# Performance work log

Measured on AMD Instinct MI355X. Metric: run time of the kernel, lower is better.

## Reference

```python
import jax, jax.numpy as jnp
import numpy as np

N_NODES = 100_000
N_EDGES = 1_000_000
VOCAB = 10_000
HID = 75
OUT = 64
BN_EPS = 1e-5


def gcn_conv(x, edge_index, W, b, n):
    # PyG GCNConv: add self-loops, symmetric deg^{-1/2} normalization, then scatter-add.
    loop = jnp.arange(n, dtype=edge_index.dtype)
    src = jnp.concatenate([edge_index[0], loop])
    dst = jnp.concatenate([edge_index[1], loop])
    deg = jax.ops.segment_sum(jnp.ones_like(src, dtype=x.dtype), dst, num_segments=n)
    dinv = jnp.where(deg > 0, jax.lax.rsqrt(deg), 0.0)
    norm = dinv[src] * dinv[dst]              # [E+N]
    h = x @ W                                  # linear before propagate (PyG order)
    msg = h[src] * norm[:, None]               # gather + per-edge scale
    out = jax.ops.segment_sum(msg, dst, num_segments=n)
    return out + b


def batch_norm(x, gamma, beta):
    # BatchNorm1d over nodes, training mode (biased variance)
    mu = jnp.mean(x, axis=0)
    var = jnp.mean(jnp.square(x - mu), axis=0)
    return (x - mu) * jax.lax.rsqrt(var + BN_EPS) * gamma + beta


def setup_inputs() -> dict:
    key = jax.random.key(0)
    ks = jax.random.split(key, 8)
    x = jax.random.randint(ks[0], (N_NODES,), 0, VOCAB, dtype=jnp.int64)
    edge_index = jax.random.randint(ks[1], (2, N_EDGES), 0, N_NODES, dtype=jnp.int64)
    emb = jax.random.normal(ks[2], (VOCAB, HID), dtype=jnp.float32)
    scale = 1.0 / np.sqrt(HID)
    Ws = jax.random.normal(ks[3], (4, HID, HID), dtype=jnp.float32) * scale
    bs = jnp.zeros((4, HID), dtype=jnp.float32)
    gammas = jnp.ones((4, HID), dtype=jnp.float32)
    betas = jnp.zeros((4, HID), dtype=jnp.float32)
    W_mu = jax.random.normal(ks[4], (HID, OUT), dtype=jnp.float32) * scale
    b_mu = jnp.zeros((OUT,), dtype=jnp.float32)
    W_logstd = jax.random.normal(ks[5], (HID, OUT), dtype=jnp.float32) * scale
    b_logstd = jnp.zeros((OUT,), dtype=jnp.float32)
    return {"x": x, "edge_index": edge_index, "emb": emb, "Ws": Ws, "bs": bs,
            "gammas": gammas, "betas": betas, "W_mu": W_mu, "b_mu": b_mu,
            "W_logstd": W_logstd, "b_logstd": b_logstd}


def reference(x, edge_index, emb, Ws, bs, gammas, betas, W_mu, b_mu, W_logstd, b_logstd):
    h = emb[x]  # [N, 75] embedding lookup
    for i in range(4):
        h = jax.nn.relu(batch_norm(gcn_conv(h, edge_index, Ws[i], bs[i], N_NODES), gammas[i], betas[i]))
    mu = gcn_conv(h, edge_index, W_mu, b_mu, N_NODES)
    logstd = gcn_conv(h, edge_index, W_logstd, b_logstd, N_NODES)
    return (mu, logstd)
```

## Files before the change

kernel.cpp:

```cpp
#include <hip/hip_runtime.h>

#define NN 100000
#define NE 1000000
#define HID 75
#define SP 80
#define OUTF 64
#define BN_EPS 1e-5f
#define KP 104

#define SCAN_ELEMS 1024
#define SCAN_NBLK ((NN + SCAN_ELEMS - 1) / SCAN_ELEMS)

typedef short bf16x8 __attribute__((ext_vector_type(8)));
typedef float f32x4  __attribute__((ext_vector_type(4)));

__device__ __forceinline__ ushort f2bf(float f) {
    unsigned u = __float_as_uint(f);
    u += 0x7FFF + ((u >> 16) & 1);
    return (ushort)(u >> 16);
}
__device__ __forceinline__ float bf_lo(unsigned u) { return __uint_as_float(u << 16); }
__device__ __forceinline__ float bf_hi(unsigned u) { return __uint_as_float(u & 0xFFFF0000u); }

__global__ void hist_kernel(const int* __restrict__ dst, int* __restrict__ hist, int E) {
    int e = blockIdx.x * blockDim.x + threadIdx.x;
    if (e < E) atomicAdd(&hist[dst[e]], 1);
}

__global__ void dinv_kernel(const int* __restrict__ hist, float* __restrict__ dinv, int n) {
    int i = blockIdx.x * blockDim.x + threadIdx.x;
    if (i < n) dinv[i] = rsqrtf((float)hist[i] + 1.0f);
}

__global__ void scan_pass1(const int* __restrict__ hist, int* __restrict__ bsum) {
    __shared__ int sdata[256];
    int base = blockIdx.x * SCAN_ELEMS;
    int t = threadIdx.x;
    int s = 0;
    #pragma unroll
    for (int k = 0; k < 4; ++k) {
        int i = base + t * 4 + k;
        if (i < NN) s += hist[i];
    }
    sdata[t] = s;
    __syncthreads();
    for (int off = 128; off > 0; off >>= 1) {
        if (t < off) sdata[t] += sdata[t + off];
        __syncthreads();
    }
    if (t == 0) bsum[blockIdx.x] = sdata[0];
}

__global__ void scan_pass2(int* __restrict__ bsum, int* __restrict__ row_ptr, int nblk) {
    if (threadIdx.x == 0) {
        int acc = 0;
        for (int i = 0; i < nblk; ++i) { int v = bsum[i]; bsum[i] = acc; acc += v; }
        row_ptr[NN] = acc;
    }
}

__global__ void scan_pass3(const int* __restrict__ hist, const int* __restrict__ bsum,
                           int* __restrict__ row_ptr) {
    __shared__ int sdata[256];
    int base = blockIdx.x * SCAN_ELEMS;
    int t = threadIdx.x;
    int v[4];
    int s = 0;
    #pragma unroll
    for (int k = 0; k < 4; ++k) {
        int i = base + t * 4 + k;
        v[k] = (i < NN) ? hist[i] : 0;
        s += v[k];
    }
    sdata[t] = s;
    __syncthreads();
    for (int off = 1; off < 256; off <<= 1) {
        int x = (t >= off) ? sdata[t - off] : 0;
        __syncthreads();
        sdata[t] += x;
        __syncthreads();
    }
    int pre = bsum[blockIdx.x] + sdata[t] - s;
    #pragma unroll
    for (int k = 0; k < 4; ++k) {
        int i = base + t * 4 + k;
        if (i < NN) { row_ptr[i] = pre; pre += v[k]; }
    }
}

__global__ void csr_fill(const int* __restrict__ src, const int* __restrict__ dst,
                         const int* __restrict__ row_ptr, int* __restrict__ cnt,
                         int* __restrict__ col, int E) {
    int e = blockIdx.x * blockDim.x + threadIdx.x;
    if (e >= E) return;
    int d = dst[e];
    int slot = row_ptr[d] + atomicAdd(&cnt[d], 1);
    col[slot] = src[e];
}

__global__ void embed_kernel(const int* __restrict__ x, const float* __restrict__ emb,
                             float* __restrict__ h) {
    int t = blockIdx.x * blockDim.x + threadIdx.x;
    if (t >= NN * SP) return;
    int node = t / SP, f = t % SP;
    h[t] = (f < HID) ? emb[x[node] * HID + f] : 0.0f;
}

template<int J, bool BNRELU>
__global__ __launch_bounds__(256, 2)
void gemm_mfma(const float* __restrict__ h, const float* __restrict__ W,
               const float* __restrict__ ab, const float* __restrict__ dinv,
               ushort* __restrict__ outb) {
    constexpr int NT = (J + 15) / 16;
    constexpr int JP = NT * 16;
    constexpr int OS = JP;
    __shared__ ushort Wl[JP * KP];
    __shared__ ushort Hl[64 * KP];
    int tl = threadIdx.x;
    int rbase = blockIdx.x * 64;
    for (int idx = tl; idx < 96 * JP; idx += 256) {
        int k = idx / JP, n = idx % JP;
        float v = (k < HID && n < J) ? W[k * J + n] : 0.0f;
        Wl[n * KP + k] = f2bf(v);
    }
    for (int idx = tl; idx < 64 * 20; idx += 256) {
        int r = idx / 20, c = idx % 20;
        int row = rbase + r; if (row >= NN) row = NN - 1;
        float4 v = reinterpret_cast<const float4*>(h + (size_t)row * SP)[c];
        if (BNRELU) {
            float4 a4 = reinterpret_cast<const float4*>(ab)[c];
            float4 c4 = reinterpret_cast<const float4*>(ab + SP)[c];
            v.x = fmaxf(fmaf(v.x, a4.x, c4.x), 0.f);
            v.y = fmaxf(fmaf(v.y, a4.y, c4.y), 0.f);
            v.z = fmaxf(fmaf(v.z, a4.z, c4.z), 0.f);
            v.w = fmaxf(fmaf(v.w, a4.w, c4.w), 0.f);
        }
        ushort4 u;
        u.x = f2bf(v.x); u.y = f2bf(v.y); u.z = f2bf(v.z); u.w = f2bf(v.w);
        *reinterpret_cast<ushort4*>(&Hl[r * KP + c * 4]) = u;
    }
    for (int idx = tl; idx < 64 * 16; idx += 256) {
        int r = idx / 16, k = 80 + (idx % 16);
        Hl[r * KP + k] = 0;
    }
    __syncthreads();
    int w = tl >> 6;
    int l = tl & 63;
    int cq = l & 15;
    int q  = l >> 4;
    f32x4 acc[NT] = {};
    #pragma unroll
    for (int ks = 0; ks < 3; ++ks) {
        int k0 = ks * 32 + q * 8;
        bf16x8 a = *reinterpret_cast<const bf16x8*>(&Hl[(w * 16 + cq) * KP + k0]);
        #pragma unroll
        for (int t = 0; t < NT; ++t) {
            bf16x8 b = *reinterpret_cast<const bf16x8*>(&Wl[(t * 16 + cq) * KP + k0]);
            acc[t] = __builtin_amdgcn_mfma_f32_16x16x32_bf16(a, b, acc[t], 0, 0, 0);
        }
    }
    int r0 = rbase + w * 16 + q * 4;
    #pragma unroll
    for (int r = 0; r < 4; ++r) {
        int grow = r0 + r;
        if (grow < NN) {
            float d = dinv[grow];
            ushort* orow = outb + (size_t)grow * OS;
            #pragma unroll
            for (int t = 0; t < NT; ++t)
                orow[t * 16 + cq] = f2bf(acc[t][r] * d);
        }
    }
}

#define ACCUM(W) \
    a0 += bf_lo(W.x); a1 += bf_hi(W.x); a2 += bf_lo(W.y); a3 += bf_hi(W.y);

__global__ void gather75(const int* __restrict__ row_ptr, const int* __restrict__ col,
                         const uint2* __restrict__ hWb, const float* __restrict__ dinv,
                         float* __restrict__ agg) {
    int t = blockIdx.x * 256 + threadIdx.x;
    if (t >= NN * 20) return;
    int n = t / 20, c = t % 20;
    int beg = row_ptr[n], end = row_ptr[n + 1];
    uint2 v = hWb[(size_t)n * 20 + c];
    float a0 = bf_lo(v.x), a1 = bf_hi(v.x), a2 = bf_lo(v.y), a3 = bf_hi(v.y);
    int e = beg;
    for (; e + 3 < end; e += 4) {
        int s0 = col[e], s1 = col[e + 1], s2 = col[e + 2], s3 = col[e + 3];
        uint2 w0 = hWb[(size_t)s0 * 20 + c];
        uint2 w1 = hWb[(size_t)s1 * 20 + c];
        uint2 w2 = hWb[(size_t)s2 * 20 + c];
        uint2 w3 = hWb[(size_t)s3 * 20 + c];
        ACCUM(w0) ACCUM(w1) ACCUM(w2) ACCUM(w3)
    }
    for (; e < end; ++e) {
        uint2 w0 = hWb[(size_t)col[e] * 20 + c];
        ACCUM(w0)
    }
    float d = dinv[n];
    reinterpret_cast<float4*>(agg)[(size_t)n * 20 + c] =
        make_float4(a0 * d, a1 * d, a2 * d, a3 * d);
}

__global__ void gather64(const int* __restrict__ row_ptr, const int* __restrict__ col,
                         const uint2* __restrict__ hWb, const float* __restrict__ dinv,
                         const float* __restrict__ bias, float* __restrict__ out) {
    int t = blockIdx.x * 256 + threadIdx.x;
    int n = t / 16, c = t % 16;
    int beg = row_ptr[n], end = row_ptr[n + 1];
    uint2 v = hWb[(size_t)n * 16 + c];
    float a0 = bf_lo(v.x), a1 = bf_hi(v.x), a2 = bf_lo(v.y), a3 = bf_hi(v.y);
    int e = beg;
    for (; e + 3 < end; e += 4) {
        int s0 = col[e], s1 = col[e + 1], s2 = col[e + 2], s3 = col[e + 3];
        uint2 w0 = hWb[(size_t)s0 * 16 + c];
        uint2 w1 = hWb[(size_t)s1 * 16 + c];
        uint2 w2 = hWb[(size_t)s2 * 16 + c];
        uint2 w3 = hWb[(size_t)s3 * 16 + c];
        ACCUM(w0) ACCUM(w1) ACCUM(w2) ACCUM(w3)
    }
    for (; e < end; ++e) {
        uint2 w0 = hWb[(size_t)col[e] * 16 + c];
        ACCUM(w0)
    }
    float d = dinv[n];
    float4 b = *reinterpret_cast<const float4*>(bias + c * 4);
    reinterpret_cast<float4*>(out)[(size_t)n * 16 + c] =
        make_float4(fmaf(a0, d, b.x), fmaf(a1, d, b.y), fmaf(a2, d, b.z), fmaf(a3, d, b.w));
}

__global__ void stats_kernel(const float* __restrict__ agg, float* __restrict__ stats) {
    __shared__ float ssum[SP], ssq[SP];
    if (threadIdx.x < SP) { ssum[threadIdx.x] = 0.f; ssq[threadIdx.x] = 0.f; }
    __syncthreads();
    int gtid = blockIdx.x * blockDim.x + threadIdx.x;
    int T = gridDim.x * blockDim.x;
    int c = gtid % 20;
    int r = gtid / 20;
    int rstep = T / 20;
    float4 s = make_float4(0.f, 0.f, 0.f, 0.f), q = make_float4(0.f, 0.f, 0.f, 0.f);
    for (; r < NN; r += rstep) {
        float4 v = reinterpret_cast<const float4*>(agg)[r * 20 + c];
        s.x += v.x; s.y += v.y; s.z += v.z; s.w += v.w;
        q.x += v.x * v.x; q.y += v.y * v.y; q.z += v.z * v.z; q.w += v.w * v.w;
    }
    atomicAdd(&ssum[c * 4 + 0], s.x); atomicAdd(&ssum[c * 4 + 1], s.y);
    atomicAdd(&ssum[c * 4 + 2], s.z); atomicAdd(&ssum[c * 4 + 3], s.w);
    atomicAdd(&ssq[c * 4 + 0], q.x); atomicAdd(&ssq[c * 4 + 1], q.y);
    atomicAdd(&ssq[c * 4 + 2], q.z); atomicAdd(&ssq[c * 4 + 3], q.w);
    __syncthreads();
    if (threadIdx.x < SP) {
        atomicAdd(&stats[threadIdx.x], ssum[threadIdx.x]);
        atomicAdd(&stats[SP + threadIdx.x], ssq[threadIdx.x]);
    }
}

__global__ void bn_finalize(const float* __restrict__ stats, const float* __restrict__ gamma,
                            const float* __restrict__ beta, float* __restrict__ ab) {
    int f = threadIdx.x;
    if (f >= SP) return;
    float a = 0.f, cc = 0.f;
    if (f < HID) {
        float mu = stats[f] * (1.0f / NN);
        float var = stats[SP + f] * (1.0f / NN) - mu * mu;
        a = gamma[f] * rsqrtf(var + BN_EPS);
        cc = beta[f] - mu * a;
    }
    ab[f] = a;
    ab[SP + f] = cc;
}

extern "C" void kernel_launch(void* const* d_in, const int* in_sizes, int n_in,
                              void* d_out, int out_size, void* d_ws, size_t ws_size,
                              hipStream_t stream) {
    const int*   x      = (const int*)d_in[0];
    const int*   ei     = (const int*)d_in[1];
    const float* emb    = (const float*)d_in[2];
    const float* Ws     = (const float*)d_in[3];
    const float* gammas = (const float*)d_in[5];
    const float* betas  = (const float*)d_in[6];
    const float* W_mu   = (const float*)d_in[7];
    const float* b_mu   = (const float*)d_in[8];
    const float* W_ls   = (const float*)d_in[9];
    const float* b_ls   = (const float*)d_in[10];
    float* out = (float*)d_out;

    const int E = in_sizes[1] / 2;
    const int* src = ei;
    const int* dst = ei + E;

    char* ws = (char*)d_ws;
    float*  dinv    = (float*) (ws + 0);
    float*  stats   = (float*) (ws + 400000);
    float*  ab      = (float*) (ws + 400640);
    int*    hist    = (int*)   (ws + 401408);
    int*    row_ptr = (int*)   (ws + 801408);
    int*    cnt     = (int*)   (ws + 1201536);
    int*    bsum    = (int*)   (ws + 1601536);
    int*    col     = (int*)   (ws + 1602048);
    float*  hA      = (float*) (ws + 5602048);
    ushort* hBb     = (ushort*)(ws + 37602048);

    hipMemsetAsync(hist, 0, NN * sizeof(int), stream);
    hist_kernel<<<(E + 255) / 256, 256, 0, stream>>>(dst, hist, E);
    dinv_kernel<<<(NN + 255) / 256, 256, 0, stream>>>(hist, dinv, NN);
    scan_pass1<<<SCAN_NBLK, 256, 0, stream>>>(hist, bsum);
    scan_pass2<<<1, 64, 0, stream>>>(bsum, row_ptr, SCAN_NBLK);
    scan_pass3<<<SCAN_NBLK, 256, 0, stream>>>(hist, bsum, row_ptr);
    hipMemsetAsync(cnt, 0, NN * sizeof(int), stream);
    csr_fill<<<(E + 255) / 256, 256, 0, stream>>>(src, dst, row_ptr, cnt, col, E);

    embed_kernel<<<(NN * SP + 255) / 256, 256, 0, stream>>>(x, emb, hA);

    for (int layer = 0; layer < 4; ++layer) {
        const float* W = Ws + (size_t)layer * HID * HID;
        if (layer == 0)
            gemm_mfma<HID, false><<<(NN + 63) / 64, 256, 0, stream>>>(hA, W, ab, dinv, hBb);
        else
            gemm_mfma<HID, true><<<(NN + 63) / 64, 256, 0, stream>>>(hA, W, ab, dinv, hBb);
        gather75<<<(NN * 20 + 255) / 256, 256, 0, stream>>>(row_ptr, col, (const uint2*)hBb, dinv, hA);
        hipMemsetAsync(stats, 0, 2 * SP * sizeof(float), stream);
        stats_kernel<<<640, 256, 0, stream>>>(hA, stats);
        bn_finalize<<<1, 128, 0, stream>>>(stats, gammas + layer * HID, betas + layer * HID, ab);
    }

    gemm_mfma<OUTF, true><<<(NN + 63) / 64, 256, 0, stream>>>(hA, W_mu, ab, dinv, hBb);
    gather64<<<(NN * 16) / 256, 256, 0, stream>>>(row_ptr, col, (const uint2*)hBb, dinv, b_mu, out);

    float* out2 = out + (size_t)NN * OUTF;
    gemm_mfma<OUTF, true><<<(NN + 63) / 64, 256, 0, stream>>>(hA, W_ls, ab, dinv, hBb);
    gather64<<<(NN * 16) / 256, 256, 0, stream>>>(row_ptr, col, (const uint2*)hBb, dinv, b_ls, out2);
}
```

Before: 628.7 us.

## Degree-sort nodes for gather load balance and fuse mu/logstd heads

Builds a permutation of nodes bucketed by in-degree (a counting sort on capped degree) and has the gather kernels visit nodes in that order, so lanes in a wavefront work on rows of similar length and divergence drops. It also merges the two output heads into one GEMM with a 128-wide concatenated weight and a single 128-feature gather that writes both outputs, removing one GEMM and one gather pass. The cost is a few extra setup kernels, scattered output writes under the permutation, and a wider intermediate buffer.

```diff
diff --git a/kernel.cpp b/kernel.cpp
--- a/kernel.cpp
+++ b/kernel.cpp
@@ -96,6 +96,42 @@
     int d = dst[e];
     int slot = row_ptr[d] + atomicAdd(&cnt[d], 1);
     col[slot] = src[e];
+}
+
+__global__ void deg_hist_kernel(const int* __restrict__ hist, int* __restrict__ dh) {
+    __shared__ int lh[64];
+    if (threadIdx.x < 64) lh[threadIdx.x] = 0;
+    __syncthreads();
+    int i = blockIdx.x * 256 + threadIdx.x;
+    if (i < NN) atomicAdd(&lh[min(hist[i], 63)], 1);
+    __syncthreads();
+    if (threadIdx.x < 64 && lh[threadIdx.x]) atomicAdd(&dh[threadIdx.x], lh[threadIdx.x]);
+}
+
+__global__ void deg_scan_kernel(const int* __restrict__ dh, int* __restrict__ doff) {
+    if (threadIdx.x == 0) {
+        int acc = 0;
+        for (int d = 0; d < 64; ++d) { doff[d] = acc; acc += dh[d]; }
+    }
+}
+
+__global__ void perm_fill_kernel(const int* __restrict__ hist, int* __restrict__ doff,
+                                 int* __restrict__ perm) {
+    __shared__ int lcnt[64];
+    __shared__ int gbase[64];
+    if (threadIdx.x < 64) lcnt[threadIdx.x] = 0;
+    __syncthreads();
+    int i = blockIdx.x * 256 + threadIdx.x;
+    int d = 0, lrank = 0;
+    bool act = (i < NN);
+    if (act) { d = min(hist[i], 63); lrank = atomicAdd(&lcnt[d], 1); }
+    __syncthreads();
+    if (threadIdx.x < 64) {
+        int c = lcnt[threadIdx.x];
+        gbase[threadIdx.x] = c ? atomicAdd(&doff[threadIdx.x], c) : 0;
+    }
+    __syncthreads();
+    if (act) perm[gbase[d] + lrank] = i;
 }
 
 __global__ void embed_kernel(const int* __restrict__ x, const float* __restrict__ emb,
@@ -173,15 +209,81 @@
     }
 }
 
+__global__ __launch_bounds__(256, 2)
+void gemm_mfma_dual(const float* __restrict__ h, const float* __restrict__ Wmu,
+                    const float* __restrict__ Wls, const float* __restrict__ ab,
+                    const float* __restrict__ dinv, ushort* __restrict__ outb) {
+    constexpr int NT = 8;
+    constexpr int JP = 128;
+    __shared__ ushort Wl[JP * KP];
+    __shared__ ushort Hl[64 * KP];
+    int tl = threadIdx.x;
+    int rbase = blockIdx.x * 64;
+    for (int idx = tl; idx < 96 * JP; idx += 256) {
+        int k = idx / JP, n = idx % JP;
+        float v = 0.f;
+        if (k < HID) v = (n < 64) ? Wmu[k * 64 + n] : Wls[k * 64 + (n - 64)];
+        Wl[n * KP + k] = f2bf(v);
+    }
+    for (int idx = tl; idx < 64 * 20; idx += 256) {
+        int r = idx / 20, c = idx % 20;
+        int row = rbase + r; if (row >= NN) row = NN - 1;
+        float4 v = reinterpret_cast<const float4*>(h + (size_t)row * SP)[c];
+        float4 a4 = reinterpret_cast<const float4*>(ab)[c];
+        float4 c4 = reinterpret_cast<const float4*>(ab + SP)[c];
+        v.x = fmaxf(fmaf(v.x, a4.x, c4.x), 0.f);
+        v.y = fmaxf(fmaf(v.y, a4.y, c4.y), 0.f);
+        v.z = fmaxf(fmaf(v.z, a4.z, c4.z), 0.f);
+        v.w = fmaxf(fmaf(v.w, a4.w, c4.w), 0.f);
+        ushort4 u;
+        u.x = f2bf(v.x); u.y = f2bf(v.y); u.z = f2bf(v.z); u.w = f2bf(v.w);
+        *reinterpret_cast<ushort4*>(&Hl[r * KP + c * 4]) = u;
+    }
+    for (int idx = tl; idx < 64 * 16; idx += 256) {
+        int r = idx / 16, k = 80 + (idx % 16);
+        Hl[r * KP + k] = 0;
+    }
+    __syncthreads();
+    int w = tl >> 6;
+    int l = tl & 63;
+    int cq = l & 15;
+    int q  = l >> 4;
+    f32x4 acc[NT] = {};
+    #pragma unroll
+    for (int ks = 0; ks < 3; ++ks) {
+        int k0 = ks * 32 + q * 8;
+        bf16x8 a = *reinterpret_cast<const bf16x8*>(&Hl[(w * 16 + cq) * KP + k0]);
+        #pragma unroll
+        for (int t = 0; t < NT; ++t) {
+            bf16x8 b = *reinterpret_cast<const bf16x8*>(&Wl[(t * 16 + cq) * KP + k0]);
+            acc[t] = __builtin_amdgcn_mfma_f32_16x16x32_bf16(a, b, acc[t], 0, 0, 0);
+        }
+    }
+    int r0 = rbase + w * 16 + q * 4;
+    #pragma unroll
+    for (int r = 0; r < 4; ++r) {
+        int grow = r0 + r;
+        if (grow < NN) {
+            float d = dinv[grow];
+            ushort* orow = outb + (size_t)grow * 128;
+            #pragma unroll
+            for (int t = 0; t < NT; ++t)
+                orow[t * 16 + cq] = f2bf(acc[t][r] * d);
+        }
+    }
+}
+
 #define ACCUM(W) \
     a0 += bf_lo(W.x); a1 += bf_hi(W.x); a2 += bf_lo(W.y); a3 += bf_hi(W.y);
 
 __global__ void gather75(const int* __restrict__ row_ptr, const int* __restrict__ col,
+                         const int* __restrict__ perm,
                          const uint2* __restrict__ hWb, const float* __restrict__ dinv,
                          float* __restrict__ agg) {
     int t = blockIdx.x * 256 + threadIdx.x;
     if (t >= NN * 20) return;
-    int n = t / 20, c = t % 20;
+    int n = perm[t / 20];
+    int c = t % 20;
     int beg = row_ptr[n], end = row_ptr[n + 1];
     uint2 v = hWb[(size_t)n * 20 + c];
     float a0 = bf_lo(v.x), a1 = bf_hi(v.x), a2 = bf_lo(v.y), a3 = bf_hi(v.y);
@@ -203,30 +305,36 @@
         make_float4(a0 * d, a1 * d, a2 * d, a3 * d);
 }
 
-__global__ void gather64(const int* __restrict__ row_ptr, const int* __restrict__ col,
-                         const uint2* __restrict__ hWb, const float* __restrict__ dinv,
-                         const float* __restrict__ bias, float* __restrict__ out) {
+__global__ void gather128(const int* __restrict__ row_ptr, const int* __restrict__ col,
+                          const int* __restrict__ perm,
+                          const uint2* __restrict__ hWb, const float* __restrict__ dinv,
+                          const float* __restrict__ b_mu, const float* __restrict__ b_ls,
+                          float* __restrict__ out_mu, float* __restrict__ out_ls) {
     int t = blockIdx.x * 256 + threadIdx.x;
-    int n = t / 16, c = t % 16;
+    int n = perm[t >> 5];
+    int c = t & 31;
     int beg = row_ptr[n], end = row_ptr[n + 1];
-    uint2 v = hWb[(size_t)n * 16 + c];
+    uint2 v = hWb[(size_t)n * 32 + c];
     float a0 = bf_lo(v.x), a1 = bf_hi(v.x), a2 = bf_lo(v.y), a3 = bf_hi(v.y);
     int e = beg;
     for (; e + 3 < end; e += 4) {
         int s0 = col[e], s1 = col[e + 1], s2 = col[e + 2], s3 = col[e + 3];
-        uint2 w0 = hWb[(size_t)s0 * 16 + c];
-        uint2 w1 = hWb[(size_t)s1 * 16 + c];
-        uint2 w2 = hWb[(size_t)s2 * 16 + c];
-        uint2 w3 = hWb[(size_t)s3 * 16 + c];
+        uint2 w0 = hWb[(size_t)s0 * 32 + c];
+        uint2 w1 = hWb[(size_t)s1 * 32 + c];
+        uint2 w2 = hWb[(size_t)s2 * 32 + c];
+        uint2 w3 = hWb[(size_t)s3 * 32 + c];
         ACCUM(w0) ACCUM(w1) ACCUM(w2) ACCUM(w3)
     }
     for (; e < end; ++e) {
-        uint2 w0 = hWb[(size_t)col[e] * 16 + c];
+        uint2 w0 = hWb[(size_t)col[e] * 32 + c];
         ACCUM(w0)
     }
     float d = dinv[n];
-    float4 b = *reinterpret_cast<const float4*>(bias + c * 4);
-    reinterpret_cast<float4*>(out)[(size_t)n * 16 + c] =
+    const float* bp = (c < 16) ? (b_mu + c * 4) : (b_ls + (c - 16) * 4);
+    float* op = (c < 16) ? (out_mu + (size_t)n * 64 + c * 4)
+                         : (out_ls + (size_t)n * 64 + (c - 16) * 4);
+    float4 b = *reinterpret_cast<const float4*>(bp);
+    *reinterpret_cast<float4*>(op) =
         make_float4(fmaf(a0, d, b.x), fmaf(a1, d, b.y), fmaf(a2, d, b.z), fmaf(a3, d, b.w));
 }
 
@@ -301,6 +409,9 @@
     int*    col     = (int*)   (ws + 1602048);
     float*  hA      = (float*) (ws + 5602048);
     ushort* hBb     = (ushort*)(ws + 37602048);
+    int*    perm    = (int*)   (ws + 63202048);
+    int*    dh      = (int*)   (ws + 63602048);
+    int*    doff    = (int*)   (ws + 63602304);
 
     hipMemsetAsync(hist, 0, NN * sizeof(int), stream);
     hist_kernel<<<(E + 255) / 256, 256, 0, stream>>>(dst, hist, E);
@@ -311,6 +422,11 @@
     hipMemsetAsync(cnt, 0, NN * sizeof(int), stream);
     csr_fill<<<(E + 255) / 256, 256, 0, stream>>>(src, dst, row_ptr, cnt, col, E);
 
+    hipMemsetAsync(dh, 0, 64 * sizeof(int), stream);
+    deg_hist_kernel<<<(NN + 255) / 256, 256, 0, stream>>>(hist, dh);
+    deg_scan_kernel<<<1, 64, 0, stream>>>(dh, doff);
+    perm_fill_kernel<<<(NN + 255) / 256, 256, 0, stream>>>(hist, doff, perm);
+
     embed_kernel<<<(NN * SP + 255) / 256, 256, 0, stream>>>(x, emb, hA);
 
     for (int layer = 0; layer < 4; ++layer) {
@@ -319,16 +435,15 @@
             gemm_mfma<HID, false><<<(NN + 63) / 64, 256, 0, stream>>>(hA, W, ab, dinv, hBb);
         else
             gemm_mfma<HID, true><<<(NN + 63) / 64, 256, 0, stream>>>(hA, W, ab, dinv, hBb);
-        gather75<<<(NN * 20 + 255) / 256, 256, 0, stream>>>(row_ptr, col, (const uint2*)hBb, dinv, hA);
+        gather75<<<(NN * 20 + 255) / 256, 256, 0, stream>>>(row_ptr, col, perm,
+                                                            (const uint2*)hBb, dinv, hA);
         hipMemsetAsync(stats, 0, 2 * SP * sizeof(float), stream);
         stats_kernel<<<640, 256, 0, stream>>>(hA, stats);
         bn_finalize<<<1, 128, 0, stream>>>(stats, gammas + layer * HID, betas + layer * HID, ab);
     }
 
-    gemm_mfma<OUTF, true><<<(NN + 63) / 64, 256, 0, stream>>>(hA, W_mu, ab, dinv, hBb);
-    gather64<<<(NN * 16) / 256, 256, 0, stream>>>(row_ptr, col, (const uint2*)hBb, dinv, b_mu, out);
-
     float* out2 = out + (size_t)NN * OUTF;
-    gemm_mfma<OUTF, true><<<(NN + 63) / 64, 256, 0, stream>>>(hA, W_ls, ab, dinv, hBb);
-    gather64<<<(NN * 16) / 256, 256, 0, stream>>>(row_ptr, col, (const uint2*)hBb, dinv, b_ls, out2);
-}
+    gemm_mfma_dual<<<(NN + 63) / 64, 256, 0, stream>>>(hA, W_mu, W_ls, ab, dinv, hBb);
+    gather128<<<(NN * 32) / 256, 256, 0, stream>>>(row_ptr, col, perm, (const uint2*)hBb,
+                                                   dinv, b_mu, b_ls, out, out2);
+}
```

Result: no change. 631.1 us (+0.4%).
